# Kernel optimization log

Hardware: AMD Instinct MI355X
Metric: run time of the kernel (lower is better)

Reference implementation:

```python
import jax, jax.numpy as jnp
import numpy as np

D_MODEL = 512
N_HEADS = 8
D_K = D_MODEL // N_HEADS  # 64
MAX_LEN = 5000


def _positional_encoding(d_model, max_len):
    pe = np.zeros((max_len, d_model), dtype=np.float32)
    position = np.arange(max_len, dtype=np.float32)[:, None]
    div_term = np.exp(np.arange(0, d_model, 2, dtype=np.float32) * (-np.log(10000.0) / d_model))
    pe[:, 0::2] = np.sin(position * div_term)
    pe[:, 1::2] = np.cos(position * div_term)
    return jnp.asarray(pe)


def _layer_norm(x, gamma, beta, eps):
    mu = jnp.mean(x, axis=-1, keepdims=True)
    var = jnp.mean(jnp.square(x - mu), axis=-1, keepdims=True)
    return (x - mu) * jax.lax.rsqrt(var + eps) * gamma + beta


def setup_inputs() -> dict:
    key = jax.random.key(0)
    ks = jax.random.split(key, 5)
    s = 1.0 / np.sqrt(D_MODEL)
    return {
        "x": jax.random.normal(ks[0], (4, 2048, D_MODEL), dtype=jnp.float32),
        "ln1_g": jnp.ones((D_MODEL,), jnp.float32),
        "ln1_b": jnp.zeros((D_MODEL,), jnp.float32),
        "wq": jax.random.normal(ks[1], (D_MODEL, D_MODEL), jnp.float32) * s,
        "wk": jax.random.normal(ks[2], (D_MODEL, D_MODEL), jnp.float32) * s,
        "wv": jax.random.normal(ks[3], (D_MODEL, D_MODEL), jnp.float32) * s,
        "wfc": jax.random.normal(ks[4], (D_MODEL, D_MODEL), jnp.float32) * s,
        "ln2_g": jnp.ones((D_MODEL,), jnp.float32),
        "ln2_b": jnp.zeros((D_MODEL,), jnp.float32),
    }


def reference(x, ln1_g, ln1_b, wq, wk, wv, wfc, ln2_g, ln2_b):
    B, T, D = x.shape
    residual0 = x
    # outer pre-norm (nn.LayerNorm default eps=1e-5)
    h = _layer_norm(x, ln1_g, ln1_b, 1e-5)
    # sinusoidal positional encoding
    h = h + _positional_encoding(D_MODEL, MAX_LEN)[:T]
    residual1 = h
    # projections -> [B, H, T, d]
    q = (h @ wq).reshape(B, T, N_HEADS, D_K).transpose(0, 2, 1, 3)
    k = (h @ wk).reshape(B, T, N_HEADS, D_K).transpose(0, 2, 1, 3)
    v = (h @ wv).reshape(B, T, N_HEADS, D_K).transpose(0, 2, 1, 3)
    scale = 1.0 / np.sqrt(D_K).astype(np.float32)
    attn = jnp.einsum("bhqd,bhkd->bhqk", q * scale, k)
    causal = jnp.tril(jnp.ones((T, T), dtype=bool))  # subsequent mask
    attn = jnp.where(causal, attn, jnp.float32(-1e9))
    attn = jax.nn.softmax(attn, axis=-1)
    o = jnp.einsum("bhqk,bhkd->bhqd", attn, v)
    o = o.transpose(0, 2, 1, 3).reshape(B, T, D)
    o = o @ wfc
    # inner post-attention residual + LayerNorm (eps=1e-6)
    h2 = _layer_norm(o + residual1, ln2_g, ln2_b, 1e-6)
    return h2 + residual0
```

## Files before the change

kernel.cpp:

```cpp
#include <hip/hip_runtime.h>
#include <hip/hip_bf16.h>

#define B_ 4
#define T_ 2048
#define D_ 512
#define H_ 8
#define M_ (B_*T_)

typedef __attribute__((ext_vector_type(8))) short short8;
typedef __attribute__((ext_vector_type(4))) short short4v;
typedef __attribute__((ext_vector_type(4))) float float4v;
typedef unsigned short bf16_t;

__device__ __forceinline__ bf16_t f2bf(float f) {
  unsigned int u = __builtin_bit_cast(unsigned int, f);
  unsigned int r = (u + 0x7fffu + ((u >> 16) & 1u)) >> 16;
  return (bf16_t)r;
}

__device__ __forceinline__ float waveReduceSum(float v) {
#pragma unroll
  for (int m = 32; m >= 1; m >>= 1) v += __shfl_xor(v, m, 64);
  return v;
}

__global__ __launch_bounds__(256) void wconv_kernel(
    const float* __restrict__ wq, const float* __restrict__ wk,
    const float* __restrict__ wv, const float* __restrict__ wfc,
    bf16_t* __restrict__ wqkvT, bf16_t* __restrict__ wfcT) {
  for (int idx = blockIdx.x * 256 + threadIdx.x; idx < 1048576; idx += 262144) {
    if (idx < 786432) {
      int n = idx >> 9, k = idx & 511;
      const float* src = (n < 512) ? wq : ((n < 1024) ? wk : wv);
      int c = n & 511;
      wqkvT[idx] = f2bf(src[k * 512 + c]);
    } else {
      int j = idx - 786432;
      int n = j >> 9, k = j & 511;
      wfcT[j] = f2bf(wfc[k * 512 + n]);
    }
  }
}

__global__ __launch_bounds__(256) void ln1_pe_kernel(
    const float* __restrict__ x, const float* __restrict__ g,
    const float* __restrict__ bb, float* __restrict__ h_f32,
    bf16_t* __restrict__ h_bf16) {
  int wave = threadIdx.x >> 6, lane = threadIdx.x & 63;
  int row = blockIdx.x * 4 + wave;
  int pos = row & (T_ - 1);
  const float* xr = x + (size_t)row * D_;
  int c0 = lane * 8;
  float v[8];
  float4 a = *(const float4*)(xr + c0);
  float4 b4 = *(const float4*)(xr + c0 + 4);
  v[0]=a.x; v[1]=a.y; v[2]=a.z; v[3]=a.w;
  v[4]=b4.x; v[5]=b4.y; v[6]=b4.z; v[7]=b4.w;
  float s = 0.f;
#pragma unroll
  for (int j = 0; j < 8; ++j) s += v[j];
  s = waveReduceSum(s);
  float mu = s * (1.f / 512.f);
  float q = 0.f;
#pragma unroll
  for (int j = 0; j < 8; ++j) { float d = v[j] - mu; q += d * d; }
  q = waveReduceSum(q);
  float rstd = rsqrtf(q * (1.f / 512.f) + 1e-5f);
  float* hr = h_f32 + (size_t)row * D_;
  bf16_t* hb = h_bf16 + (size_t)row * D_;
#pragma unroll
  for (int j = 0; j < 8; ++j) {
    int col = c0 + j;
    float hn = (v[j] - mu) * rstd * g[col] + bb[col];
    int i2 = (col >> 1) << 1;
    float dt = __expf((float)i2 * (-9.2103403719761836f / 512.0f));
    float ang = (float)pos * dt;
    float pe = (col & 1) ? __cosf(ang) : __sinf(ang);
    float hv = hn + pe;
    hr[col] = hv;
    hb[col] = f2bf(hv);
  }
}

template <int N_COLS, bool OUT_BF16>
__global__ __launch_bounds__(256) void gemm_kernel(
    const bf16_t* __restrict__ A, const bf16_t* __restrict__ Bt,
    void* __restrict__ Cv) {
  __shared__ __align__(16) bf16_t As[64 * 72];
  __shared__ __align__(16) bf16_t Bs[64 * 72];
  const int m0 = blockIdx.y * 64;
  const int n0 = blockIdx.x * 64;
  const int tid = threadIdx.x;
  const int wave = tid >> 6, lane = tid & 63;
  const int ln = lane & 15, quad = lane >> 4;
  float4v acc[4];
  float4v z = {0.f, 0.f, 0.f, 0.f};
#pragma unroll
  for (int i = 0; i < 4; ++i) acc[i] = z;

  for (int k0 = 0; k0 < 512; k0 += 64) {
#pragma unroll
    for (int it = 0; it < 2; ++it) {
      int cid = tid + it * 256;
      int row = cid >> 3, cb = (cid & 7) << 3;
      short8 av = *(const short8*)(A + (size_t)(m0 + row) * 512 + k0 + cb);
      *(short8*)(As + row * 72 + cb) = av;
      short8 bv = *(const short8*)(Bt + (size_t)(n0 + row) * 512 + k0 + cb);
      *(short8*)(Bs + row * 72 + cb) = bv;
    }
    __syncthreads();
#pragma unroll
    for (int c = 0; c < 2; ++c) {
      short8 af = *(short8*)(As + (wave * 16 + ln) * 72 + c * 32 + quad * 8);
#pragma unroll
      for (int nt = 0; nt < 4; ++nt) {
        short8 bf = *(short8*)(Bs + (nt * 16 + ln) * 72 + c * 32 + quad * 8);
        acc[nt] = __builtin_amdgcn_mfma_f32_16x16x32_bf16(af, bf, acc[nt], 0, 0, 0);
      }
    }
    __syncthreads();
  }
#pragma unroll
  for (int nt = 0; nt < 4; ++nt) {
#pragma unroll
    for (int r = 0; r < 4; ++r) {
      int row = m0 + wave * 16 + quad * 4 + r;
      int col = n0 + nt * 16 + ln;
      if (OUT_BF16)
        ((bf16_t*)Cv)[(size_t)row * N_COLS + col] = f2bf(acc[nt][r]);
      else
        ((float*)Cv)[(size_t)row * N_COLS + col] = acc[nt][r];
    }
  }
}

__global__ __launch_bounds__(256) void attn_kernel(const bf16_t* __restrict__ qk,
                                                   const bf16_t* __restrict__ vT,
                                                   bf16_t* __restrict__ out) {
  __shared__ __align__(16) bf16_t Ks[2][64 * 72];
  __shared__ __align__(16) bf16_t Vs[2][64 * 72];
  __shared__ __align__(16) bf16_t Ps[4][16 * 72];
  const int bx = blockIdx.x;
  const int qt = 31 - (bx >> 5);
  const int bh = bx & 31;
  const int b = bh >> 3, h = bh & 7;
  const int tid = threadIdx.x;
  const int w = tid >> 6, lane = tid & 63;
  const int ln = lane & 15, quad = lane >> 4;
  const int srow = tid >> 3;
  const int scb = (tid & 7) << 3;

  short8 qf0, qf1;
  {
    size_t qrow = ((size_t)b * T_ + qt * 64 + w * 16 + ln) * 1024 + h * 64;
    qf0 = *(const short8*)(qk + qrow + quad * 8);
    qf1 = *(const short8*)(qk + qrow + 32 + quad * 8);
  }
  float4v z = {0.f, 0.f, 0.f, 0.f};
  float4v oacc[4];
#pragma unroll
  for (int i = 0; i < 4; ++i) oacc[i] = z;
  float m_s = -1e30f, l_s = 0.f;

  const size_t kcolbase = 512 + h * 64;
  const size_t vbase = (size_t)(h * 64) * 8192 + (size_t)b * T_;

  short8 kr0, kr1, vr0, vr1;
  {
    size_t kb = ((size_t)b * T_) * 1024 + kcolbase;
    kr0 = *(const short8*)(qk + kb + (size_t)srow * 1024 + scb);
    kr1 = *(const short8*)(qk + kb + (size_t)(srow + 32) * 1024 + scb);
    vr0 = *(const short8*)(vT + vbase + (size_t)srow * 8192 + scb);
    vr1 = *(const short8*)(vT + vbase + (size_t)(srow + 32) * 8192 + scb);
  }
  *(short8*)(Ks[0] + srow * 72 + scb) = kr0;
  *(short8*)(Ks[0] + (srow + 32) * 72 + scb) = kr1;
  *(short8*)(Vs[0] + srow * 72 + scb) = vr0;
  *(short8*)(Vs[0] + (srow + 32) * 72 + scb) = vr1;
  __syncthreads();

  bf16_t* Psw = Ps[w];

  for (int kt = 0; kt <= qt; ++kt) {
    const int cur = kt & 1;
    const bool more = (kt < qt);
    if (more) {
      size_t kb = ((size_t)b * T_ + (kt + 1) * 64) * 1024 + kcolbase;
      kr0 = *(const short8*)(qk + kb + (size_t)srow * 1024 + scb);
      kr1 = *(const short8*)(qk + kb + (size_t)(srow + 32) * 1024 + scb);
      size_t vb = vbase + (kt + 1) * 64;
      vr0 = *(const short8*)(vT + vb + (size_t)srow * 8192 + scb);
      vr1 = *(const short8*)(vT + vb + (size_t)(srow + 32) * 8192 + scb);
    }
    float sv[4][4];
#pragma unroll
    for (int mt = 0; mt < 4; ++mt) {
      float4v st = z;
      short8 a0 = *(short8*)(Ks[cur] + (mt * 16 + ln) * 72 + quad * 8);
      short8 a1 = *(short8*)(Ks[cur] + (mt * 16 + ln) * 72 + 32 + quad * 8);
      st = __builtin_amdgcn_mfma_f32_16x16x32_bf16(a0, qf0, st, 0, 0, 0);
      st = __builtin_amdgcn_mfma_f32_16x16x32_bf16(a1, qf1, st, 0, 0, 0);
#pragma unroll
      for (int r = 0; r < 4; ++r) {
        float v = st[r] * 0.125f;
        if (kt == qt) {
          int kloc = mt * 16 + quad * 4 + r;
          if (kloc > w * 16 + ln) v = -1e30f;
        }
        sv[mt][r] = v;
      }
    }
    float mx = sv[0][0];
#pragma unroll
    for (int mt = 0; mt < 4; ++mt)
#pragma unroll
      for (int r = 0; r < 4; ++r) mx = fmaxf(mx, sv[mt][r]);
    mx = fmaxf(mx, __shfl_xor(mx, 16, 64));
    mx = fmaxf(mx, __shfl_xor(mx, 32, 64));
    float mn = fmaxf(m_s, mx);
    float alpha = __expf(m_s - mn);
    m_s = mn;
    float rs = 0.f;
#pragma unroll
    for (int mt = 0; mt < 4; ++mt)
#pragma unroll
      for (int r = 0; r < 4; ++r) {
        float p = __expf(sv[mt][r] - mn);
        sv[mt][r] = p;
        rs += p;
      }
    rs += __shfl_xor(rs, 16, 64);
    rs += __shfl_xor(rs, 32, 64);
    l_s = l_s * alpha + rs;
#pragma unroll
    for (int dt = 0; dt < 4; ++dt)
#pragma unroll
      for (int r = 0; r < 4; ++r) oacc[dt][r] *= alpha;
#pragma unroll
    for (int mt = 0; mt < 4; ++mt) {
      short4v p4;
#pragma unroll
      for (int r = 0; r < 4; ++r) p4[r] = (short)f2bf(sv[mt][r]);
      *(short4v*)(Psw + ln * 72 + mt * 16 + quad * 4) = p4;
    }
    short8 bp0 = *(short8*)(Psw + ln * 72 + quad * 8);
    short8 bp1 = *(short8*)(Psw + ln * 72 + 32 + quad * 8);
#pragma unroll
    for (int dt = 0; dt < 4; ++dt) {
      short8 av0 = *(short8*)(Vs[cur] + (dt * 16 + ln) * 72 + quad * 8);
      short8 av1 = *(short8*)(Vs[cur] + (dt * 16 + ln) * 72 + 32 + quad * 8);
      oacc[dt] = __builtin_amdgcn_mfma_f32_16x16x32_bf16(av0, bp0, oacc[dt], 0, 0, 0);
      oacc[dt] = __builtin_amdgcn_mfma_f32_16x16x32_bf16(av1, bp1, oacc[dt], 0, 0, 0);
    }
    if (more) {
      const int nxt = cur ^ 1;
      *(short8*)(Ks[nxt] + srow * 72 + scb) = kr0;
      *(short8*)(Ks[nxt] + (srow + 32) * 72 + scb) = kr1;
      *(short8*)(Vs[nxt] + srow * 72 + scb) = vr0;
      *(short8*)(Vs[nxt] + (srow + 32) * 72 + scb) = vr1;
    }
    __syncthreads();
  }
  float inv = 1.0f / l_s;
  size_t obase = ((size_t)b * T_ + qt * 64 + w * 16 + ln) * 512 + h * 64;
#pragma unroll
  for (int dt = 0; dt < 4; ++dt) {
    short4v o4;
#pragma unroll
    for (int r = 0; r < 4; ++r) o4[r] = (short)f2bf(oacc[dt][r] * inv);
    *(short4v*)(out + obase + dt * 16 + quad * 4) = o4;
  }
}

__global__ __launch_bounds__(256) void ln2_kernel(
    const float* __restrict__ o2, const float* __restrict__ hres,
    const float* __restrict__ x, const float* __restrict__ g,
    const float* __restrict__ bb, float* __restrict__ out) {
  int wave = threadIdx.x >> 6, lane = threadIdx.x & 63;
  int row = blockIdx.x * 4 + wave;
  size_t ro = (size_t)row * D_;
  int c0 = lane * 8;
  float t[8];
  float4 a0 = *(const float4*)(o2 + ro + c0);
  float4 a1 = *(const float4*)(o2 + ro + c0 + 4);
  float4 h0 = *(const float4*)(hres + ro + c0);
  float4 h1 = *(const float4*)(hres + ro + c0 + 4);
  t[0]=a0.x+h0.x; t[1]=a0.y+h0.y; t[2]=a0.z+h0.z; t[3]=a0.w+h0.w;
  t[4]=a1.x+h1.x; t[5]=a1.y+h1.y; t[6]=a1.z+h1.z; t[7]=a1.w+h1.w;
  float s = 0.f;
#pragma unroll
  for (int j = 0; j < 8; ++j) s += t[j];
  s = waveReduceSum(s);
  float mu = s * (1.f / 512.f);
  float q = 0.f;
#pragma unroll
  for (int j = 0; j < 8; ++j) { float d = t[j] - mu; q += d * d; }
  q = waveReduceSum(q);
  float rstd = rsqrtf(q * (1.f / 512.f) + 1e-6f);
#pragma unroll
  for (int j = 0; j < 8; ++j) {
    int col = c0 + j;
    out[ro + col] = (t[j] - mu) * rstd * g[col] + bb[col] + x[ro + col];
  }
}

extern "C" void kernel_launch(void* const* d_in, const int* in_sizes, int n_in,
                              void* d_out, int out_size, void* d_ws, size_t ws_size,
                              hipStream_t stream) {
  const float* x   = (const float*)d_in[0];
  const float* g1  = (const float*)d_in[1];
  const float* b1  = (const float*)d_in[2];
  const float* wq  = (const float*)d_in[3];
  const float* wk  = (const float*)d_in[4];
  const float* wv  = (const float*)d_in[5];
  const float* wfc = (const float*)d_in[6];
  const float* g2  = (const float*)d_in[7];
  const float* b2  = (const float*)d_in[8];
  float* out = (float*)d_out;

  char* ws = (char*)d_ws;
  const size_t O_HF32  = 0;
  const size_t O_HBF   = 16777216;
  const size_t O_WQKV  = 25165824;
  const size_t O_WFC   = 26738688;
  const size_t O_QK    = 27262976;
  const size_t O_VT    = 44040192;
  const size_t O_ATTN  = 52428800;
  const size_t O_O2    = 60817408;
  const size_t WS_NEED = 77594624;
  if (ws_size < WS_NEED) return;

  float*  h_f32 = (float*)(ws + O_HF32);
  bf16_t* h_bf  = (bf16_t*)(ws + O_HBF);
  bf16_t* wqkvT = (bf16_t*)(ws + O_WQKV);
  bf16_t* wfcT  = (bf16_t*)(ws + O_WFC);
  bf16_t* qk    = (bf16_t*)(ws + O_QK);
  bf16_t* vT    = (bf16_t*)(ws + O_VT);
  bf16_t* attn  = (bf16_t*)(ws + O_ATTN);
  float*  o2    = (float*)(ws + O_O2);

  wconv_kernel<<<dim3(1024), dim3(256), 0, stream>>>(wq, wk, wv, wfc, wqkvT, wfcT);
  ln1_pe_kernel<<<dim3(2048), dim3(256), 0, stream>>>(x, g1, b1, h_f32, h_bf);
  gemm_kernel<1024, true><<<dim3(16, 128), dim3(256), 0, stream>>>(h_bf, wqkvT, (void*)qk);
  gemm_kernel<8192, true><<<dim3(128, 8), dim3(256), 0, stream>>>(wqkvT + 1024 * 512, h_bf, (void*)vT);
  attn_kernel<<<dim3(1024), dim3(256), 0, stream>>>(qk, vT, attn);
  gemm_kernel<512, false><<<dim3(8, 128), dim3(256), 0, stream>>>(attn, wfcT, (void*)o2);
  ln2_kernel<<<dim3(2048), dim3(256), 0, stream>>>(o2, h_f32, x, g2, b2, out);
}
```

Measured before the change: 196.0 us.

## Use 128x128 GEMM tiles with direct global-to-LDS loads and XOR swizzle

GEMMs move from 64x64 to 128x128 output tiles with a 2x2 wave layout and 16 accumulators per wave. Operands are loaded straight into LDS with global_load_lds in an XOR-swizzled layout, replacing the padded register-staged copies. The attention kernel uses the same direct LDS staging and swizzle for K/V, peels the masked diagonal tile out of the loop, and folds the 1/8 score scale into the K weights during conversion. The larger tiles cut redundant operand loads and raise MFMA density, but they shrink the grid to as few as 256 blocks, which may under-fill the GPU for the smaller GEMMs.

```diff
diff --git a/kernel.cpp b/kernel.cpp
--- a/kernel.cpp
+++ b/kernel.cpp
@@ -4,8 +4,6 @@
 #define B_ 4
 #define T_ 2048
 #define D_ 512
-#define H_ 8
-#define M_ (B_*T_)
 
 typedef __attribute__((ext_vector_type(8))) short short8;
 typedef __attribute__((ext_vector_type(4))) short short4v;
@@ -22,6 +20,12 @@
 #pragma unroll
   for (int m = 32; m >= 1; m >>= 1) v += __shfl_xor(v, m, 64);
   return v;
+}
+
+__device__ __forceinline__ void gld16(const bf16_t* g, bf16_t* l) {
+  __builtin_amdgcn_global_load_lds(
+      (const __attribute__((address_space(1))) void*)g,
+      (__attribute__((address_space(3))) void*)l, 16, 0, 0);
 }
 
 __global__ __launch_bounds__(256) void wconv_kernel(
@@ -32,8 +36,9 @@
     if (idx < 786432) {
       int n = idx >> 9, k = idx & 511;
       const float* src = (n < 512) ? wq : ((n < 1024) ? wk : wv);
+      float scl = (n >= 512 && n < 1024) ? 0.125f : 1.0f;
       int c = n & 511;
-      wqkvT[idx] = f2bf(src[k * 512 + c]);
+      wqkvT[idx] = f2bf(src[k * 512 + c] * scl);
     } else {
       int j = idx - 786432;
       int n = j >> 9, k = j & 511;
@@ -82,63 +87,81 @@
   }
 }
 
-template <int N_COLS, bool OUT_BF16>
-__global__ __launch_bounds__(256) void gemm_kernel(
+template <int N_COLS, int OUT_BF16>
+__global__ __launch_bounds__(256) void gemm128_kernel(
     const bf16_t* __restrict__ A, const bf16_t* __restrict__ Bt,
     void* __restrict__ Cv) {
-  __shared__ __align__(16) bf16_t As[64 * 72];
-  __shared__ __align__(16) bf16_t Bs[64 * 72];
-  const int m0 = blockIdx.y * 64;
-  const int n0 = blockIdx.x * 64;
+  __shared__ __align__(16) bf16_t As[128 * 64];
+  __shared__ __align__(16) bf16_t Bs[128 * 64];
+  const int m0 = blockIdx.y * 128, n0 = blockIdx.x * 128;
   const int tid = threadIdx.x;
-  const int wave = tid >> 6, lane = tid & 63;
+  const int w = tid >> 6, lane = tid & 63;
   const int ln = lane & 15, quad = lane >> 4;
-  float4v acc[4];
+  const int wy = w >> 1, wx = w & 1;
+  const int sw = ln & 7;
+
+  float4v acc[4][4];
   float4v z = {0.f, 0.f, 0.f, 0.f};
 #pragma unroll
-  for (int i = 0; i < 4; ++i) acc[i] = z;
+  for (int i = 0; i < 4; ++i)
+#pragma unroll
+    for (int j = 0; j < 4; ++j) acc[i][j] = z;
 
   for (int k0 = 0; k0 < 512; k0 += 64) {
 #pragma unroll
-    for (int it = 0; it < 2; ++it) {
-      int cid = tid + it * 256;
-      int row = cid >> 3, cb = (cid & 7) << 3;
-      short8 av = *(const short8*)(A + (size_t)(m0 + row) * 512 + k0 + cb);
-      *(short8*)(As + row * 72 + cb) = av;
-      short8 bv = *(const short8*)(Bt + (size_t)(n0 + row) * 512 + k0 + cb);
-      *(short8*)(Bs + row * 72 + cb) = bv;
+    for (int i = 0; i < 4; ++i) {
+      int cbase = w * 256 + i * 64;
+      int chunk = cbase + lane;
+      int row = chunk >> 3;
+      int lb = (chunk & 7) ^ (row & 7);
+      gld16(A + (size_t)(m0 + row) * 512 + k0 + lb * 8, As + (size_t)cbase * 8);
+      gld16(Bt + (size_t)(n0 + row) * 512 + k0 + lb * 8, Bs + (size_t)cbase * 8);
     }
     __syncthreads();
 #pragma unroll
     for (int c = 0; c < 2; ++c) {
-      short8 af = *(short8*)(As + (wave * 16 + ln) * 72 + c * 32 + quad * 8);
+      short8 af[4], bf[4];
+#pragma unroll
+      for (int mt = 0; mt < 4; ++mt) {
+        int row = wy * 64 + mt * 16 + ln;
+        int pb = (c * 4 + quad) ^ sw;
+        af[mt] = *(const short8*)(As + row * 64 + pb * 8);
+      }
 #pragma unroll
       for (int nt = 0; nt < 4; ++nt) {
-        short8 bf = *(short8*)(Bs + (nt * 16 + ln) * 72 + c * 32 + quad * 8);
-        acc[nt] = __builtin_amdgcn_mfma_f32_16x16x32_bf16(af, bf, acc[nt], 0, 0, 0);
-      }
+        int row = wx * 64 + nt * 16 + ln;
+        int pb = (c * 4 + quad) ^ sw;
+        bf[nt] = *(const short8*)(Bs + row * 64 + pb * 8);
+      }
+#pragma unroll
+      for (int mt = 0; mt < 4; ++mt)
+#pragma unroll
+        for (int nt = 0; nt < 4; ++nt)
+          acc[mt][nt] = __builtin_amdgcn_mfma_f32_16x16x32_bf16(af[mt], bf[nt], acc[mt][nt], 0, 0, 0);
     }
     __syncthreads();
   }
 #pragma unroll
-  for (int nt = 0; nt < 4; ++nt) {
+  for (int mt = 0; mt < 4; ++mt)
 #pragma unroll
     for (int r = 0; r < 4; ++r) {
-      int row = m0 + wave * 16 + quad * 4 + r;
-      int col = n0 + nt * 16 + ln;
-      if (OUT_BF16)
-        ((bf16_t*)Cv)[(size_t)row * N_COLS + col] = f2bf(acc[nt][r]);
-      else
-        ((float*)Cv)[(size_t)row * N_COLS + col] = acc[nt][r];
-    }
-  }
+      int row = m0 + wy * 64 + mt * 16 + quad * 4 + r;
+#pragma unroll
+      for (int nt = 0; nt < 4; ++nt) {
+        int col = n0 + wx * 64 + nt * 16 + ln;
+        if (OUT_BF16)
+          ((bf16_t*)Cv)[(size_t)row * N_COLS + col] = f2bf(acc[mt][nt][r]);
+        else
+          ((float*)Cv)[(size_t)row * N_COLS + col] = acc[mt][nt][r];
+      }
+    }
 }
 
 __global__ __launch_bounds__(256) void attn_kernel(const bf16_t* __restrict__ qk,
                                                    const bf16_t* __restrict__ vT,
                                                    bf16_t* __restrict__ out) {
-  __shared__ __align__(16) bf16_t Ks[2][64 * 72];
-  __shared__ __align__(16) bf16_t Vs[2][64 * 72];
+  __shared__ __align__(16) bf16_t Ks[2][64 * 64];
+  __shared__ __align__(16) bf16_t Vs[2][64 * 64];
   __shared__ __align__(16) bf16_t Ps[4][16 * 72];
   const int bx = blockIdx.x;
   const int qt = 31 - (bx >> 5);
@@ -147,8 +170,7 @@
   const int tid = threadIdx.x;
   const int w = tid >> 6, lane = tid & 63;
   const int ln = lane & 15, quad = lane >> 4;
-  const int srow = tid >> 3;
-  const int scb = (tid & 7) << 3;
+  const int sw = ln & 7;
 
   short8 qf0, qf1;
   {
@@ -162,48 +184,36 @@
   for (int i = 0; i < 4; ++i) oacc[i] = z;
   float m_s = -1e30f, l_s = 0.f;
 
-  const size_t kcolbase = 512 + h * 64;
-  const size_t vbase = (size_t)(h * 64) * 8192 + (size_t)b * T_;
-
-  short8 kr0, kr1, vr0, vr1;
-  {
-    size_t kb = ((size_t)b * T_) * 1024 + kcolbase;
-    kr0 = *(const short8*)(qk + kb + (size_t)srow * 1024 + scb);
-    kr1 = *(const short8*)(qk + kb + (size_t)(srow + 32) * 1024 + scb);
-    vr0 = *(const short8*)(vT + vbase + (size_t)srow * 8192 + scb);
-    vr1 = *(const short8*)(vT + vbase + (size_t)(srow + 32) * 8192 + scb);
-  }
-  *(short8*)(Ks[0] + srow * 72 + scb) = kr0;
-  *(short8*)(Ks[0] + (srow + 32) * 72 + scb) = kr1;
-  *(short8*)(Vs[0] + srow * 72 + scb) = vr0;
-  *(short8*)(Vs[0] + (srow + 32) * 72 + scb) = vr1;
-  __syncthreads();
-
+  const bf16_t* kbase = qk + (size_t)b * T_ * 1024 + 512 + h * 64;
+  const bf16_t* vbase = vT + (size_t)(h * 64) * 8192 + (size_t)b * T_;
   bf16_t* Psw = Ps[w];
 
-  for (int kt = 0; kt <= qt; ++kt) {
-    const int cur = kt & 1;
-    const bool more = (kt < qt);
-    if (more) {
-      size_t kb = ((size_t)b * T_ + (kt + 1) * 64) * 1024 + kcolbase;
-      kr0 = *(const short8*)(qk + kb + (size_t)srow * 1024 + scb);
-      kr1 = *(const short8*)(qk + kb + (size_t)(srow + 32) * 1024 + scb);
-      size_t vb = vbase + (kt + 1) * 64;
-      vr0 = *(const short8*)(vT + vb + (size_t)srow * 8192 + scb);
-      vr1 = *(const short8*)(vT + vb + (size_t)(srow + 32) * 8192 + scb);
-    }
+  auto stage = [&](int buf, int kt) {
+#pragma unroll
+    for (int i = 0; i < 2; ++i) {
+      int cbase = w * 128 + i * 64;
+      int chunk = cbase + lane;
+      int row = chunk >> 3;
+      int lb = (chunk & 7) ^ (row & 7);
+      gld16(kbase + (size_t)(kt * 64 + row) * 1024 + lb * 8, Ks[buf] + (size_t)cbase * 8);
+      gld16(vbase + (size_t)row * 8192 + kt * 64 + lb * 8, Vs[buf] + (size_t)cbase * 8);
+    }
+  };
+
+  auto compute = [&](const bf16_t* Kc, const bf16_t* Vc, bool mask) {
     float sv[4][4];
 #pragma unroll
     for (int mt = 0; mt < 4; ++mt) {
       float4v st = z;
-      short8 a0 = *(short8*)(Ks[cur] + (mt * 16 + ln) * 72 + quad * 8);
-      short8 a1 = *(short8*)(Ks[cur] + (mt * 16 + ln) * 72 + 32 + quad * 8);
+      int row = mt * 16 + ln;
+      short8 a0 = *(const short8*)(Kc + row * 64 + ((0 + quad) ^ sw) * 8);
+      short8 a1 = *(const short8*)(Kc + row * 64 + ((4 + quad) ^ sw) * 8);
       st = __builtin_amdgcn_mfma_f32_16x16x32_bf16(a0, qf0, st, 0, 0, 0);
       st = __builtin_amdgcn_mfma_f32_16x16x32_bf16(a1, qf1, st, 0, 0, 0);
 #pragma unroll
       for (int r = 0; r < 4; ++r) {
-        float v = st[r] * 0.125f;
-        if (kt == qt) {
+        float v = st[r];
+        if (mask) {
           int kloc = mt * 16 + quad * 4 + r;
           if (kloc > w * 16 + ln) v = -1e30f;
         }
@@ -247,20 +257,24 @@
     short8 bp1 = *(short8*)(Psw + ln * 72 + 32 + quad * 8);
 #pragma unroll
     for (int dt = 0; dt < 4; ++dt) {
-      short8 av0 = *(short8*)(Vs[cur] + (dt * 16 + ln) * 72 + quad * 8);
-      short8 av1 = *(short8*)(Vs[cur] + (dt * 16 + ln) * 72 + 32 + quad * 8);
+      int row = dt * 16 + ln;
+      short8 av0 = *(const short8*)(Vc + row * 64 + ((0 + quad) ^ sw) * 8);
+      short8 av1 = *(const short8*)(Vc + row * 64 + ((4 + quad) ^ sw) * 8);
       oacc[dt] = __builtin_amdgcn_mfma_f32_16x16x32_bf16(av0, bp0, oacc[dt], 0, 0, 0);
       oacc[dt] = __builtin_amdgcn_mfma_f32_16x16x32_bf16(av1, bp1, oacc[dt], 0, 0, 0);
     }
-    if (more) {
-      const int nxt = cur ^ 1;
-      *(short8*)(Ks[nxt] + srow * 72 + scb) = kr0;
-      *(short8*)(Ks[nxt] + (srow + 32) * 72 + scb) = kr1;
-      *(short8*)(Vs[nxt] + srow * 72 + scb) = vr0;
-      *(short8*)(Vs[nxt] + (srow + 32) * 72 + scb) = vr1;
-    }
+  };
+
+  stage(0, 0);
+  __syncthreads();
+  for (int kt = 0; kt < qt; ++kt) {
+    int cur = kt & 1;
+    stage(cur ^ 1, kt + 1);
+    compute(Ks[cur], Vs[cur], false);
     __syncthreads();
   }
+  compute(Ks[qt & 1], Vs[qt & 1], true);
+
   float inv = 1.0f / l_s;
   size_t obase = ((size_t)b * T_ + qt * 64 + w * 16 + ln) * 512 + h * 64;
 #pragma unroll
@@ -341,9 +355,9 @@
 
   wconv_kernel<<<dim3(1024), dim3(256), 0, stream>>>(wq, wk, wv, wfc, wqkvT, wfcT);
   ln1_pe_kernel<<<dim3(2048), dim3(256), 0, stream>>>(x, g1, b1, h_f32, h_bf);
-  gemm_kernel<1024, true><<<dim3(16, 128), dim3(256), 0, stream>>>(h_bf, wqkvT, (void*)qk);
-  gemm_kernel<8192, true><<<dim3(128, 8), dim3(256), 0, stream>>>(wqkvT + 1024 * 512, h_bf, (void*)vT);
+  gemm128_kernel<1024, 1><<<dim3(8, 64), dim3(256), 0, stream>>>(h_bf, wqkvT, (void*)qk);
+  gemm128_kernel<8192, 1><<<dim3(64, 4), dim3(256), 0, stream>>>(wqkvT + 1024 * 512, h_bf, (void*)vT);
   attn_kernel<<<dim3(1024), dim3(256), 0, stream>>>(qk, vT, attn);
-  gemm_kernel<512, false><<<dim3(8, 128), dim3(256), 0, stream>>>(attn, wfcT, (void*)o2);
+  gemm128_kernel<512, 0><<<dim3(4, 64), dim3(256), 0, stream>>>(attn, wfcT, (void*)o2);
   ln2_kernel<<<dim3(2048), dim3(256), 0, stream>>>(o2, h_f32, x, g2, b2, out);
 }
```

Result: no change. 196.9 us (+0.5%).
